# Kernel optimization log

Measured on AMD Instinct MI355X. Metric: run time of the kernel, lower is better.

Reference implementation:

```python
import jax, jax.numpy as jnp
import numpy as np

B, C, W, H = 2, 64, 96, 96
C8 = C // 8


def setup_inputs() -> dict:
    key = jax.random.key(0)
    ks = jax.random.split(key, 8)
    return {
        "x": jax.random.normal(ks[0], (B, C, W, H), dtype=jnp.float32),
        "Wq": jax.random.normal(ks[1], (C8, C), dtype=jnp.float32) * 0.05,
        "bq": jax.random.normal(ks[2], (C8,), dtype=jnp.float32) * 0.05,
        "Wk": jax.random.normal(ks[3], (C8, C), dtype=jnp.float32) * 0.05,
        "bk": jax.random.normal(ks[4], (C8,), dtype=jnp.float32) * 0.05,
        "Wv": jax.random.normal(ks[5], (C, C), dtype=jnp.float32) * 0.05,
        "bv": jax.random.normal(ks[6], (C,), dtype=jnp.float32) * 0.05,
        "gamma": jax.random.normal(ks[7], (1,), dtype=jnp.float32),
    }


def reference(x, Wq, bq, Wk, bk, Wv, bv, gamma):
    b, c, w, h = x.shape
    n = w * h
    xf = x.reshape(b, c, n)  # [B, C, N]
    # 1x1 convs are channel-mixing matmuls over flattened spatial dim
    q = jnp.einsum('oc,bcn->bno', Wq, xf) + bq          # [B, N, C//8] (proj_query, permuted)
    k = jnp.einsum('oc,bcn->bon', Wk, xf) + bk[:, None]  # [B, C//8, N] (proj_key)
    energy = jnp.einsum('bno,bom->bnm', q, k)            # [B, N, N]
    # torch softmax over dim=1 (the query index), NOT the usual dim=-1
    attn = jax.nn.softmax(energy, axis=1)                # [B, N, N]
    v = jnp.einsum('oc,bcn->bon', Wv, xf) + bv[:, None]  # [B, C, N]
    # bmm(V, attn.permute(0,2,1)): out[b,c,m] = sum_n V[b,c,n] * attn[b,m,n]
    out = jnp.einsum('bcn,bmn->bcm', v, attn).reshape(b, c, w, h)
    return gamma * out + x
```

## Files before the change

kernel.cpp:

```cpp
#include <hip/hip_runtime.h>
#include <math.h>

#define NN 9216
#define LOG2E 1.4426950408889634f

typedef __attribute__((ext_vector_type(8))) __bf16 bf16x8;
typedef __attribute__((ext_vector_type(16))) float f32x16;
typedef __attribute__((ext_vector_type(4))) unsigned int u32x4;

#define MFMA32(a,b,c) __builtin_amdgcn_mfma_f32_32x32x16_bf16(a,b,c,0,0,0)

#if __has_builtin(__builtin_amdgcn_exp2f)
#define EXP2(x) __builtin_amdgcn_exp2f(x)
#else
#define EXP2(x) exp2f(x)
#endif

__device__ __forceinline__ bf16x8 zero8() {
    bf16x8 z;
    #pragma unroll
    for (int i = 0; i < 8; i++) z[i] = (__bf16)0.0f;
    return z;
}

__device__ __forceinline__ unsigned int pk2(float a, float b) {
    unsigned short ua = __builtin_bit_cast(unsigned short, (__bf16)a);
    unsigned short ub = __builtin_bit_cast(unsigned short, (__bf16)b);
    return (unsigned int)ua | ((unsigned int)ub << 16);
}

__device__ __forceinline__ void plane_swap(unsigned int &a, unsigned int &b) {
    asm("v_permlane32_swap_b32 %0, %1" : "+v"(a), "+v"(b));
}

#define OFF_QB 0
#define OFF_KB 294912
#define OFF_VB 589824
#define OFF_VF 2949120
#define OFF_DP 5308416
#define OFF_PARTS 5308416
#define WS_NEED 24182784ULL

__global__ __launch_bounds__(256) void qkv_kernel(
    const float* __restrict__ x,
    const float* __restrict__ Wq, const float* __restrict__ bq,
    const float* __restrict__ Wk, const float* __restrict__ bk,
    const float* __restrict__ Wv, const float* __restrict__ bv,
    __bf16* __restrict__ QB, __bf16* __restrict__ KB, __bf16* __restrict__ VB)
{
    __shared__ float wsh[1024], bsh[16];
    int tid = threadIdx.x;
    int z = blockIdx.z, b = blockIdx.y;
    if (z == 0) {
        for (int i = tid; i < 512; i += 256) { wsh[i] = Wq[i]; wsh[512+i] = Wk[i]; }
        if (tid < 8)  { bsh[tid] = bq[tid]; bsh[8+tid] = bk[tid]; }
    } else {
        for (int i = tid; i < 512; i += 256) wsh[i] = Wv[(z-1)*512 + i];
        if (tid < 8)  bsh[tid] = bv[(z-1)*8 + tid];
    }
    __syncthreads();

    int n = blockIdx.x * 256 + tid;

    float xc[64];
    #pragma unroll
    for (int c = 0; c < 64; c++) xc[c] = x[((size_t)(b*64 + c))*NN + n];

    if (z == 0) {
        float q[8], k[8];
        #pragma unroll
        for (int o = 0; o < 8; o++) { q[o] = bsh[o]; k[o] = bsh[8+o]; }
        #pragma unroll
        for (int c = 0; c < 64; c++) {
            float xv = xc[c];
            #pragma unroll
            for (int o = 0; o < 8; o++) {
                q[o] = fmaf(wsh[o*64+c], xv, q[o]);
                k[o] = fmaf(wsh[512+o*64+c], xv, k[o]);
            }
        }
        bf16x8 qv, kv;
        #pragma unroll
        for (int o = 0; o < 8; o++) {
            qv[o] = (__bf16)(q[o] * LOG2E);
            kv[o] = (__bf16)k[o];
        }
        *(bf16x8*)(QB + ((size_t)b*NN + n)*8) = qv;
        *(bf16x8*)(KB + ((size_t)b*NN + n)*8) = kv;
    } else {
        float v[8];
        #pragma unroll
        for (int o = 0; o < 8; o++) v[o] = bsh[o];
        #pragma unroll
        for (int c = 0; c < 64; c++) {
            float xv = xc[c];
            #pragma unroll
            for (int o = 0; o < 8; o++) v[o] = fmaf(wsh[o*64+c], xv, v[o]);
        }
        #pragma unroll
        for (int o = 0; o < 8; o++)
            VB[((size_t)(b*64 + (z-1)*8 + o))*NN + n] = (__bf16)v[o];
    }
}

__global__ __launch_bounds__(256) void stats_kernel(
    const __bf16* __restrict__ QB, const __bf16* __restrict__ KB,
    float* __restrict__ Dp)
{
    __shared__ float Dl[4][32];
    int tid = threadIdx.x;
    int lane = tid & 63, w = tid >> 6;
    int l31 = lane & 31, h = lane >> 5;
    int b = blockIdx.y, z = blockIdx.z;
    int n0 = blockIdx.x * 32;

    f32x16 Z16;
    #pragma unroll
    for (int r = 0; r < 16; r++) Z16[r] = 0.0f;

    bf16x8 kf = zero8();
    if (lane < 32)
        kf = *(const bf16x8*)(KB + ((size_t)b*NN + n0 + l31)*8);

    float Dacc[16];
    #pragma unroll
    for (int r = 0; r < 16; r++) Dacc[r] = 0.0f;

    const __bf16* Qb = QB + (size_t)b*NN*8;
    int mbase = z*2304 + w*576;
    for (int it = 0; it < 18; it++) {
        bf16x8 qf = zero8();
        if (lane < 32)
            qf = *(const bf16x8*)(Qb + (size_t)(mbase + it*32 + l31)*8);
        f32x16 e = MFMA32(kf, qf, Z16);
        #pragma unroll
        for (int r = 0; r < 16; r++) Dacc[r] += EXP2(e[r]);
    }
    #pragma unroll
    for (int r = 0; r < 16; r++) {
        #pragma unroll
        for (int mask = 1; mask < 32; mask <<= 1)
            Dacc[r] += __shfl_xor(Dacc[r], mask);
    }
    if (l31 == 0) {
        #pragma unroll
        for (int r = 0; r < 16; r++)
            Dl[w][(r&3) + 8*(r>>2) + 4*h] = Dacc[r];
    }
    __syncthreads();
    if (tid < 32)
        Dp[((size_t)(z*2 + b))*NN + n0 + tid] =
            Dl[0][tid] + Dl[1][tid] + Dl[2][tid] + Dl[3][tid];
}

__global__ __launch_bounds__(256) void foldvf_kernel(
    const float* __restrict__ Dp, const float* __restrict__ gamma_p,
    const __bf16* __restrict__ VB, __bf16* __restrict__ VF)
{
    __shared__ float Rl[64];
    int tid = threadIdx.x;
    int b = blockIdx.y, tg = blockIdx.x;
    int n0 = tg * 64;
    if (tid < 64) {
        float d = 0.0f;
        #pragma unroll
        for (int zz = 0; zz < 4; zz++)
            d += Dp[((size_t)(zz*2 + b))*NN + n0 + tid];
        Rl[tid] = gamma_p[0] / d;
    }
    __syncthreads();

    #pragma unroll
    for (int i = 0; i < 2; i++) {
        int p = tid + i*256;
        int chunk = p >> 6, lane = p & 63;
        int c  = (chunk & 1)*32 + (lane & 31);
        int nl = ((chunk >> 2) & 1)*32 + ((chunk >> 1) & 1)*16 + (lane >> 5)*8;
        bf16x8 v = *(const bf16x8*)(VB + ((size_t)(b*64 + c))*NN + n0 + nl);
        bf16x8 ov;
        #pragma unroll
        for (int j = 0; j < 8; j++)
            ov[j] = (__bf16)((float)v[j] * Rl[nl + j]);
        *(bf16x8*)(VF + (((size_t)(b*144 + tg))*8 + chunk)*512 + lane*8) = ov;
    }
}

__global__ __launch_bounds__(256) void init_kernel(
    const float* __restrict__ x, float* __restrict__ out)
{
    int i = blockIdx.x*256 + threadIdx.x;
    ((float4*)out)[i] = ((const float4*)x)[i];
}

__global__ __launch_bounds__(256) void pv_kernel(
    const __bf16* __restrict__ QB, const __bf16* __restrict__ KB,
    const __bf16* __restrict__ VF, float* __restrict__ out,
    __bf16* __restrict__ parts)
{
    int tid = threadIdx.x;
    int lane = tid & 63, w = tid >> 6;
    int l31 = lane & 31, h = lane >> 5;
    int b = blockIdx.y, s = blockIdx.z;
    int mw = blockIdx.x * 128 + w * 32;

    f32x16 Z16;
    #pragma unroll
    for (int r = 0; r < 16; r++) Z16[r] = 0.0f;

    bf16x8 qf = zero8();
    if (lane < 32)
        qf = *(const bf16x8*)(QB + ((size_t)b*NN + mw + l31)*8);

    f32x16 acc[2];
    acc[0] = Z16; acc[1] = Z16;

    const __bf16* kbase = KB + ((size_t)b*NN + s*1152)*8;
    const __bf16* vbase = VF + ((size_t)(b*144 + s*18))*8*512;

    bf16x8 kc0 = zero8(), kc1 = zero8(), kn0 = zero8(), kn1 = zero8();
    if (lane < 32) {
        kc0 = *(const bf16x8*)(kbase + l31*8);
        kc1 = *(const bf16x8*)(kbase + (32 + l31)*8);
    }
    bf16x8 vf0, vf1, vf2, vf3, vf4, vf5, vf6, vf7;
    {
        const __bf16* vp = vbase + lane*8;
        vf0 = *(const bf16x8*)(vp + 0*512); vf1 = *(const bf16x8*)(vp + 1*512);
        vf2 = *(const bf16x8*)(vp + 2*512); vf3 = *(const bf16x8*)(vp + 3*512);
        vf4 = *(const bf16x8*)(vp + 4*512); vf5 = *(const bf16x8*)(vp + 5*512);
        vf6 = *(const bf16x8*)(vp + 6*512); vf7 = *(const bf16x8*)(vp + 7*512);
    }

    for (int t = 0; t < 18; t++) {
        f32x16 e0 = MFMA32(kc0, qf, Z16);
        f32x16 e1 = MFMA32(kc1, qf, Z16);

        if (t < 17) {
            const __bf16* knp = kbase + (t+1)*512;
            if (lane < 32) {
                kn0 = *(const bf16x8*)(knp + l31*8);
                kn1 = *(const bf16x8*)(knp + (32 + l31)*8);
            }
        }

        bf16x8 pa[2][2];
        #pragma unroll
        for (int nt = 0; nt < 2; nt++) {
            const f32x16& e = nt ? e1 : e0;
            float pf[16];
            #pragma unroll
            for (int r = 0; r < 16; r++) pf[r] = EXP2(e[r]);
            unsigned int u[8];
            #pragma unroll
            for (int q = 0; q < 8; q++) u[q] = pk2(pf[2*q], pf[2*q+1]);
            plane_swap(u[0], u[2]); plane_swap(u[1], u[3]);
            plane_swap(u[4], u[6]); plane_swap(u[5], u[7]);
            u32x4 t0 = {u[0], u[1], u[2], u[3]};
            u32x4 t1 = {u[4], u[5], u[6], u[7]};
            pa[nt][0] = __builtin_bit_cast(bf16x8, t0);
            pa[nt][1] = __builtin_bit_cast(bf16x8, t1);
        }

        __builtin_amdgcn_s_setprio(1);
        acc[0] = MFMA32(pa[0][0], vf0, acc[0]);
        acc[1] = MFMA32(pa[0][0], vf1, acc[1]);
        acc[0] = MFMA32(pa[0][1], vf2, acc[0]);
        acc[1] = MFMA32(pa[0][1], vf3, acc[1]);
        acc[0] = MFMA32(pa[1][0], vf4, acc[0]);
        acc[1] = MFMA32(pa[1][0], vf5, acc[1]);
        acc[0] = MFMA32(pa[1][1], vf6, acc[0]);
        acc[1] = MFMA32(pa[1][1], vf7, acc[1]);
        __builtin_amdgcn_s_setprio(0);

        if (t < 17) {
            const __bf16* vp = vbase + (t+1)*4096 + lane*8;
            vf0 = *(const bf16x8*)(vp + 0*512); vf1 = *(const bf16x8*)(vp + 1*512);
            vf2 = *(const bf16x8*)(vp + 2*512); vf3 = *(const bf16x8*)(vp + 3*512);
            vf4 = *(const bf16x8*)(vp + 4*512); vf5 = *(const bf16x8*)(vp + 5*512);
            vf6 = *(const bf16x8*)(vp + 6*512); vf7 = *(const bf16x8*)(vp + 7*512);
        }
        kc0 = kn0; kc1 = kn1;
    }

    if (parts != nullptr) {
        __bf16* pp = parts + ((size_t)(s*2 + b))*64*NN;
        #pragma unroll
        for (int ct = 0; ct < 2; ct++) {
            int c = ct*32 + l31;
            __bf16* row = pp + (size_t)c*NN + mw + 4*h;
            #pragma unroll
            for (int q = 0; q < 4; q++) {
                uint2 v2;
                v2.x = pk2(acc[ct][4*q],   acc[ct][4*q+1]);
                v2.y = pk2(acc[ct][4*q+2], acc[ct][4*q+3]);
                *(uint2*)(row + q*8) = v2;
            }
        }
    } else {
        #pragma unroll
        for (int ct = 0; ct < 2; ct++) {
            int c = ct*32 + l31;
            #pragma unroll
            for (int r = 0; r < 16; r++) {
                int m = mw + (r&3) + 8*(r>>2) + 4*h;
                atomicAdd(out + ((size_t)(b*64 + c))*NN + m, (float)acc[ct][r]);
            }
        }
    }
}

__global__ __launch_bounds__(256) void reduce_kernel(
    const float* __restrict__ x, const __bf16* __restrict__ parts,
    float* __restrict__ out)
{
    size_t f0 = ((size_t)blockIdx.x*256 + threadIdx.x) * 8;
    float o[8];
    float4 a = *(const float4*)(x + f0);
    float4 c = *(const float4*)(x + f0 + 4);
    o[0]=a.x; o[1]=a.y; o[2]=a.z; o[3]=a.w;
    o[4]=c.x; o[5]=c.y; o[6]=c.z; o[7]=c.w;
    #pragma unroll
    for (int sIdx = 0; sIdx < 8; sIdx++) {
        bf16x8 p = *(const bf16x8*)(parts + (size_t)sIdx*(128*NN) + f0);
        #pragma unroll
        for (int j = 0; j < 8; j++) o[j] += (float)p[j];
    }
    float4 r0 = make_float4(o[0],o[1],o[2],o[3]);
    float4 r1 = make_float4(o[4],o[5],o[6],o[7]);
    *(float4*)(out + f0) = r0;
    *(float4*)(out + f0 + 4) = r1;
}

extern "C" void kernel_launch(void* const* d_in, const int* in_sizes, int n_in,
                              void* d_out, int out_size, void* d_ws, size_t ws_size,
                              hipStream_t stream) {
    const float* x     = (const float*)d_in[0];
    const float* Wq    = (const float*)d_in[1];
    const float* bq    = (const float*)d_in[2];
    const float* Wk    = (const float*)d_in[3];
    const float* bk    = (const float*)d_in[4];
    const float* Wv    = (const float*)d_in[5];
    const float* bv    = (const float*)d_in[6];
    const float* gamma = (const float*)d_in[7];
    float* out = (float*)d_out;
    char* ws   = (char*)d_ws;

    __bf16* QB = (__bf16*)(ws + OFF_QB);
    __bf16* KB = (__bf16*)(ws + OFF_KB);
    __bf16* VB = (__bf16*)(ws + OFF_VB);
    __bf16* VF = (__bf16*)(ws + OFF_VF);
    float*  Dp = (float*)(ws + OFF_DP);

    qkv_kernel<<<dim3(36, 2, 9), 256, 0, stream>>>(x, Wq, bq, Wk, bk, Wv, bv, QB, KB, VB);
    stats_kernel<<<dim3(288, 2, 4), 256, 0, stream>>>(QB, KB, Dp);
    foldvf_kernel<<<dim3(144, 2), 256, 0, stream>>>(Dp, gamma, VB, VF);

    if (ws_size >= WS_NEED) {
        __bf16* parts = (__bf16*)(ws + OFF_PARTS);
        pv_kernel<<<dim3(72, 2, 8), 256, 0, stream>>>(QB, KB, VF, out, parts);
        reduce_kernel<<<dim3(576), 256, 0, stream>>>(x, parts, out);
    } else {
        init_kernel<<<dim3(1152), 256, 0, stream>>>(x, out);
        pv_kernel<<<dim3(72, 2, 8), 256, 0, stream>>>(QB, KB, VF, out, nullptr);
    }
}
```

Baseline: 102.3 us.

## Stage V and K tiles through double-buffered LDS via global_load_lds

Result: no change. 101.3 us (-1.0%).

```diff
diff --git a/kernel.cpp b/kernel.cpp
--- a/kernel.cpp
+++ b/kernel.cpp
@@ -31,6 +31,12 @@
 
 __device__ __forceinline__ void plane_swap(unsigned int &a, unsigned int &b) {
     asm("v_permlane32_swap_b32 %0, %1" : "+v"(a), "+v"(b));
+}
+
+__device__ __forceinline__ void cp16(void* lds, const void* g) {
+    __builtin_amdgcn_global_load_lds(
+        (const __attribute__((address_space(1))) unsigned int*)g,
+        (__attribute__((address_space(3))) unsigned int*)lds, 16, 0, 0);
 }
 
 #define OFF_QB 0
@@ -197,6 +203,9 @@
     const __bf16* __restrict__ VF, float* __restrict__ out,
     __bf16* __restrict__ parts)
 {
+    __shared__ __bf16 vbuf[2][4096];
+    __shared__ __bf16 klin[2][512];
+
     int tid = threadIdx.x;
     int lane = tid & 63, w = tid >> 6;
     int l31 = lane & 31, h = lane >> 5;
@@ -217,31 +226,30 @@
     const __bf16* kbase = KB + ((size_t)b*NN + s*1152)*8;
     const __bf16* vbase = VF + ((size_t)(b*144 + s*18))*8*512;
 
-    bf16x8 kc0 = zero8(), kc1 = zero8(), kn0 = zero8(), kn1 = zero8();
-    if (lane < 32) {
-        kc0 = *(const bf16x8*)(kbase + l31*8);
-        kc1 = *(const bf16x8*)(kbase + (32 + l31)*8);
-    }
-    bf16x8 vf0, vf1, vf2, vf3, vf4, vf5, vf6, vf7;
-    {
-        const __bf16* vp = vbase + lane*8;
-        vf0 = *(const bf16x8*)(vp + 0*512); vf1 = *(const bf16x8*)(vp + 1*512);
-        vf2 = *(const bf16x8*)(vp + 2*512); vf3 = *(const bf16x8*)(vp + 3*512);
-        vf4 = *(const bf16x8*)(vp + 4*512); vf5 = *(const bf16x8*)(vp + 5*512);
-        vf6 = *(const bf16x8*)(vp + 6*512); vf7 = *(const bf16x8*)(vp + 7*512);
-    }
+#define STAGE(bi, stq) do {                                                   \
+    const __bf16* tile_ = vbase + (size_t)(stq)*4096;                         \
+    cp16((char*)vbuf[bi] + w*1024,        tile_ + (w*64 + lane)*8);           \
+    cp16((char*)vbuf[bi] + 4096 + w*1024, tile_ + (256 + w*64 + lane)*8);     \
+    if (w == 0)                                                               \
+        cp16((char*)klin[bi], kbase + ((size_t)(stq)*64 + lane)*8);           \
+} while (0)
+
+    STAGE(0, 0);
 
     for (int t = 0; t < 18; t++) {
-        f32x16 e0 = MFMA32(kc0, qf, Z16);
-        f32x16 e1 = MFMA32(kc1, qf, Z16);
-
+        int bi = t & 1;
+        __syncthreads();
         if (t < 17) {
-            const __bf16* knp = kbase + (t+1)*512;
-            if (lane < 32) {
-                kn0 = *(const bf16x8*)(knp + l31*8);
-                kn1 = *(const bf16x8*)(knp + (32 + l31)*8);
-            }
-        }
+            if (bi == 0) STAGE(1, t+1); else STAGE(0, t+1);
+        }
+
+        bf16x8 kfr0 = zero8(), kfr1 = zero8();
+        if (lane < 32) {
+            kfr0 = *(const bf16x8*)(klin[bi] + l31*8);
+            kfr1 = *(const bf16x8*)(klin[bi] + (32 + l31)*8);
+        }
+        f32x16 e0 = MFMA32(kfr0, qf, Z16);
+        f32x16 e1 = MFMA32(kfr1, qf, Z16);
 
         bf16x8 pa[2][2];
         #pragma unroll
@@ -262,24 +270,12 @@
         }
 
         __builtin_amdgcn_s_setprio(1);
-        acc[0] = MFMA32(pa[0][0], vf0, acc[0]);
-        acc[1] = MFMA32(pa[0][0], vf1, acc[1]);
-        acc[0] = MFMA32(pa[0][1], vf2, acc[0]);
-        acc[1] = MFMA32(pa[0][1], vf3, acc[1]);
-        acc[0] = MFMA32(pa[1][0], vf4, acc[0]);
-        acc[1] = MFMA32(pa[1][0], vf5, acc[1]);
-        acc[0] = MFMA32(pa[1][1], vf6, acc[0]);
-        acc[1] = MFMA32(pa[1][1], vf7, acc[1]);
+        #pragma unroll
+        for (int chunk = 0; chunk < 8; chunk++) {
+            bf16x8 bfr = *(const bf16x8*)((char*)vbuf[bi] + chunk*1024 + lane*16);
+            acc[chunk & 1] = MFMA32(pa[chunk >> 2][(chunk >> 1) & 1], bfr, acc[chunk & 1]);
+        }
         __builtin_amdgcn_s_setprio(0);
-
-        if (t < 17) {
-            const __bf16* vp = vbase + (t+1)*4096 + lane*8;
-            vf0 = *(const bf16x8*)(vp + 0*512); vf1 = *(const bf16x8*)(vp + 1*512);
-            vf2 = *(const bf16x8*)(vp + 2*512); vf3 = *(const bf16x8*)(vp + 3*512);
-            vf4 = *(const bf16x8*)(vp + 4*512); vf5 = *(const bf16x8*)(vp + 5*512);
-            vf6 = *(const bf16x8*)(vp + 6*512); vf7 = *(const bf16x8*)(vp + 7*512);
-        }
-        kc0 = kn0; kc1 = kn1;
     }
 
     if (parts != nullptr) {
```
